# Performance work log

Hardware: AMD Instinct MI355X
Metric: run time of the kernel (lower is better)

## Reference

```python
import jax, jax.numpy as jnp
import numpy as np

LN_EPS = 1e-12


def setup_inputs() -> dict:
    key = jax.random.key(0)
    ks = jax.random.split(key, 5)
    E, H, I = 8, 768, 3072
    T = 2048  # tokens per expert (capacity-balanced)
    N = E * T
    return {
        "hidden_states": jax.random.normal(ks[0], (N, H), jnp.float32),
        "w1": jax.random.normal(ks[1], (E, H, I), jnp.float32) * (H ** -0.5),
        "b1": jax.random.normal(ks[2], (E, I), jnp.float32) * 0.02,
        "w2": jax.random.normal(ks[3], (E, I, H), jnp.float32) * (I ** -0.5),
        "b2": jax.random.normal(ks[4], (E, H), jnp.float32) * 0.02,
        "ln_gamma": jnp.ones((H,), jnp.float32),
        "ln_beta": jnp.zeros((H,), jnp.float32),
        "tokens_per_expert": T,
    }


def reference(hidden_states, w1, b1, w2, b2, ln_gamma, ln_beta, tokens_per_expert):
    E = w1.shape[0]
    N, H = hidden_states.shape
    # tokens are pre-sorted by expert; equal capacity per expert -> grouped GEMM
    x = hidden_states.reshape(E, tokens_per_expert, H)  # [E, T, H]
    # dense1 + exact GELU (BERT ACT2FN['gelu'])
    inter = jax.nn.gelu(jnp.einsum("eth,ehi->eti", x, w1) + b1[:, None, :],
                        approximate=False)  # [E, T, I]
    # dense2
    out = jnp.einsum("eti,eih->eth", inter, w2) + b2[:, None, :]  # [E, T, H]
    # dropout is identity in eval mode; residual + LayerNorm
    y = out.reshape(N, H) + hidden_states
    mean = jnp.mean(y, axis=-1, keepdims=True)
    var = jnp.mean(jnp.square(y - mean), axis=-1, keepdims=True)
    return (y - mean) * jax.lax.rsqrt(var + LN_EPS) * ln_gamma + ln_beta
```

## Files before the change

kernel.cpp:

```cpp
#include <hip/hip_runtime.h>
#include <hip/hip_bf16.h>
#include <math.h>

#define E_   8
#define H_   768
#define I_   3072
#define T_   2048
#define NTOK (E_ * T_)

typedef __attribute__((ext_vector_type(8))) short bf16x8;
typedef __attribute__((ext_vector_type(4))) float f32x4;

typedef __attribute__((address_space(3))) void lds_void;
typedef const __attribute__((address_space(1))) void gl_void;

__device__ __forceinline__ void gload16(const void* g, void* l) {
  __builtin_amdgcn_global_load_lds((gl_void*)g, (lds_void*)l, 16, 0, 0);
}

#define FENCE() asm volatile("" ::: "memory")
#define BAR()                         \
  do {                                \
    FENCE();                          \
    __builtin_amdgcn_s_barrier();     \
    FENCE();                          \
  } while (0)
#define VMWAIT(n) asm volatile("s_waitcnt vmcnt(" #n ")" ::: "memory")

#define MFMA16(a, b, c) __builtin_amdgcn_mfma_f32_16x16x32_bf16(a, b, c, 0, 0, 0)

__device__ __forceinline__ float gelu_fast(float v) {
  float inner = v * fmaf(v * v, 0.044715f, 1.0f);
  float e = __builtin_amdgcn_exp2f(inner * -2.3022082f);
  return v * __builtin_amdgcn_rcpf(1.0f + e);
}

__global__ __launch_bounds__(256) void cvt_bf16_kernel(
    const float* __restrict__ in, __hip_bfloat16* __restrict__ out) {
  int i = (blockIdx.x * 256 + threadIdx.x) * 4;
  float4 v = *(const float4*)(in + i);
  __align__(8) __hip_bfloat16 t[4];
  t[0] = __float2bfloat16(v.x);
  t[1] = __float2bfloat16(v.y);
  t[2] = __float2bfloat16(v.z);
  t[3] = __float2bfloat16(v.w);
  *(ushort4*)(out + i) = *(const ushort4*)t;
}

__global__ __launch_bounds__(256) void transpose_cvt_kernel(
    const float* __restrict__ src, __hip_bfloat16* __restrict__ dst,
    int R, int C) {
  __shared__ __hip_bfloat16 tile[64][65];
  int e  = blockIdx.z;
  int c0 = blockIdx.x * 64;
  int r0 = blockIdx.y * 64;
  const float* s = src + (size_t)e * R * C;
  __hip_bfloat16* d = dst + (size_t)e * R * C;
  int tx = threadIdx.x & 63, ty = threadIdx.x >> 6;
#pragma unroll
  for (int r = ty; r < 64; r += 4)
    tile[r][tx] = __float2bfloat16(s[(size_t)(r0 + r) * C + c0 + tx]);
  __syncthreads();
#pragma unroll
  for (int r = ty; r < 64; r += 4)
    d[(size_t)(c0 + r) * R + r0 + tx] = tile[tx][r];
}

template <int K, int N, int BN, bool GELU>
__global__ __launch_bounds__(512, 2) void gemm2p_kernel(
    const __hip_bfloat16* __restrict__ A,
    const __hip_bfloat16* __restrict__ B,
    const float* __restrict__ bias,
    __hip_bfloat16* __restrict__ out) {
  constexpr int MT = T_ / 256;
  constexpr int NT = N / BN;
  constexpr int KT = K / 64;
  constexpr int NF = BN / 64;
  constexpr int WCW = BN / 4;
  constexpr int BPASS = BN / 64;

  __shared__ __hip_bfloat16 sA[2][2][128][64];
  __shared__ __hip_bfloat16 sB[2][BN][64];

  int nwg = gridDim.x;
  int b0  = blockIdx.x;
  int bid = (b0 & 7) * (nwg >> 3) + (b0 >> 3);

  int e   = bid / (MT * NT);
  int rr_ = bid % (MT * NT);
  int bm  = rr_ / NT;
  int bn  = rr_ % NT;

  const __hip_bfloat16* Ae = A + (size_t)e * T_ * K + (size_t)bm * 256 * K;
  const __hip_bfloat16* Be = B + (size_t)e * N  * K + (size_t)bn * BN * K;

  int tid  = threadIdx.x;
  int lane = tid & 63;
  int wid  = tid >> 6;
  int wr   = wid >> 2;
  int wc   = wid & 3;
  int l15  = lane & 15;
  int l16h = lane >> 4;

  int i0 = tid, i1 = 512 + tid;
  int lr0 = i0 >> 3, c80 = i0 & 7, cg0 = c80 ^ (lr0 & 7);
  int lr1 = i1 >> 3, c81 = i1 & 7, cg1 = c81 ^ (lr1 & 7);
  int rA0 = ((lr0 >> 6) << 7) | (lr0 & 63);
  int rA1 = ((lr1 >> 6) << 7) | (lr1 & 63);

  auto stageA = [&](int buf, int h, int kt) {
    const __hip_bfloat16* g = Ae + (size_t)kt * 64;
    gload16(g + (size_t)(rA0 | (h << 6)) * K + cg0 * 8, &sA[buf][h][lr0][c80 * 8]);
    gload16(g + (size_t)(rA1 | (h << 6)) * K + cg1 * 8, &sA[buf][h][lr1][c81 * 8]);
  };
  auto stageB = [&](int buf, int kt) {
    const __hip_bfloat16* g = Be + (size_t)kt * 64;
#pragma unroll
    for (int q = 0; q < BPASS; ++q) {
      int idx = q * 512 + tid;
      int lr = idx >> 3, c8 = idx & 7;
      int cg = c8 ^ (lr & 7);
      gload16(g + (size_t)lr * K + cg * 8, &sB[buf][lr][c8 * 8]);
    }
  };

  int laBase = wr * 64 + l15;
  int lbBase = wc * WCW + l15;
  int s7   = l15 & 7;
  int cgr0 = ((0 | l16h) ^ s7) * 8;
  int cgr1 = ((4 | l16h) ^ s7) * 8;

  f32x4 acc[8][NF] = {};
  bf16x8 af[4][2], bfv[NF][2];

  stageA(0, 0, 0);
  stageB(0, 0);
  stageA(0, 1, 0);

  auto ktile = [&](int kt, int p, bool pf) {
    VMWAIT(2);
    BAR();
#pragma unroll
    for (int mf = 0; mf < 4; ++mf) {
      int la = laBase + mf * 16;
      af[mf][0] = *(const bf16x8*)&sA[p][0][la][cgr0];
      af[mf][1] = *(const bf16x8*)&sA[p][0][la][cgr1];
    }
#pragma unroll
    for (int nf = 0; nf < NF; ++nf) {
      int lb = lbBase + nf * 16;
      bfv[nf][0] = *(const bf16x8*)&sB[p][lb][cgr0];
      bfv[nf][1] = *(const bf16x8*)&sB[p][lb][cgr1];
    }
    if (pf) {
      stageA(p ^ 1, 0, kt + 1);
      stageB(p ^ 1, kt + 1);
    }
    __builtin_amdgcn_s_setprio(1);
#pragma unroll
    for (int mf = 0; mf < 4; ++mf)
#pragma unroll
      for (int nf = 0; nf < NF; ++nf) {
        acc[mf][nf] = MFMA16(af[mf][0], bfv[nf][0], acc[mf][nf]);
        acc[mf][nf] = MFMA16(af[mf][1], bfv[nf][1], acc[mf][nf]);
      }
    __builtin_amdgcn_s_setprio(0);
    if (pf) {
      if constexpr (BN == 256) { VMWAIT(6); } else { VMWAIT(5); }
    } else {
      VMWAIT(0);
    }
    BAR();
#pragma unroll
    for (int mf = 0; mf < 4; ++mf) {
      int la = laBase + mf * 16;
      af[mf][0] = *(const bf16x8*)&sA[p][1][la][cgr0];
      af[mf][1] = *(const bf16x8*)&sA[p][1][la][cgr1];
    }
    if (pf) stageA(p ^ 1, 1, kt + 1);
    __builtin_amdgcn_s_setprio(1);
#pragma unroll
    for (int mf = 0; mf < 4; ++mf)
#pragma unroll
      for (int nf = 0; nf < NF; ++nf) {
        acc[4 + mf][nf] = MFMA16(af[mf][0], bfv[nf][0], acc[4 + mf][nf]);
        acc[4 + mf][nf] = MFMA16(af[mf][1], bfv[nf][1], acc[4 + mf][nf]);
      }
    __builtin_amdgcn_s_setprio(0);
  };

  int p = 0;
  for (int kt = 0; kt < KT - 1; ++kt) {
    ktile(kt, p, true);
    p ^= 1;
  }
  ktile(KT - 1, p, false);

  const float* be = bias + (size_t)e * N + bn * BN;
  __hip_bfloat16* oe =
      out + (size_t)e * T_ * N + (size_t)(bm * 256) * N + bn * BN;
  int r4 = l16h * 4;
#pragma unroll
  for (int mi = 0; mi < 8; ++mi) {
    int mh = mi >> 2, mf = mi & 3;
    int rowb = wr * 128 + mh * 64 + mf * 16 + r4;
#pragma unroll
    for (int nf = 0; nf < NF; ++nf) {
      int cc   = wc * WCW + nf * 16 + l15;
      float bv = be[cc];
#pragma unroll
      for (int r = 0; r < 4; ++r) {
        float v = acc[mi][nf][r] + bv;
        if (GELU) v = gelu_fast(v);
        oe[(size_t)(rowb + r) * N + cc] = __float2bfloat16(v);
      }
    }
  }
}

__global__ __launch_bounds__(256) void ln_kernel(
    const __hip_bfloat16* __restrict__ yraw, const float* __restrict__ x,
    const float* __restrict__ gamma, const float* __restrict__ beta,
    float* __restrict__ out) {
  int row  = blockIdx.x;
  int tid  = threadIdx.x;
  int lane = tid & 63, wid = tid >> 6;
  const __hip_bfloat16* yr = yraw + (size_t)row * H_;
  const float* xr = x + (size_t)row * H_;

  float v[3];
  float s = 0.f, s2 = 0.f;
#pragma unroll
  for (int j = 0; j < 3; ++j) {
    int c   = tid + j * 256;
    float t = __bfloat162float(yr[c]) + xr[c];
    v[j] = t;
    s += t;
    s2 += t * t;
  }
#pragma unroll
  for (int o = 32; o > 0; o >>= 1) {
    s  += __shfl_down(s, o);
    s2 += __shfl_down(s2, o);
  }
  __shared__ float ls[4], ls2[4];
  if (lane == 0) { ls[wid] = s; ls2[wid] = s2; }
  __syncthreads();
  float tot  = ls[0] + ls[1] + ls[2] + ls[3];
  float tot2 = ls2[0] + ls2[1] + ls2[2] + ls2[3];
  float mean = tot * (1.0f / 768.0f);
  float var  = tot2 * (1.0f / 768.0f) - mean * mean;
  float inv  = rsqrtf(var + 1e-12f);
  float* orow = out + (size_t)row * H_;
#pragma unroll
  for (int j = 0; j < 3; ++j) {
    int c = tid + j * 256;
    orow[c] = (v[j] - mean) * inv * gamma[c] + beta[c];
  }
}

extern "C" void kernel_launch(void* const* d_in, const int* in_sizes, int n_in,
                              void* d_out, int out_size, void* d_ws,
                              size_t ws_size, hipStream_t stream) {
  const float* x     = (const float*)d_in[0];
  const float* w1    = (const float*)d_in[1];
  const float* b1    = (const float*)d_in[2];
  const float* w2    = (const float*)d_in[3];
  const float* b2    = (const float*)d_in[4];
  const float* gamma = (const float*)d_in[5];
  const float* beta  = (const float*)d_in[6];
  float* out = (float*)d_out;

  char* ws = (char*)d_ws;
  __hip_bfloat16* w1t   = (__hip_bfloat16*)(ws);
  __hip_bfloat16* w2t   = (__hip_bfloat16*)(ws + 37748736);
  __hip_bfloat16* x_bf  = (__hip_bfloat16*)(ws + 75497472);
  __hip_bfloat16* inter = (__hip_bfloat16*)(ws + 100663296);
  __hip_bfloat16* yraw  = x_bf;

  cvt_bf16_kernel<<<(NTOK * H_) / (256 * 4), 256, 0, stream>>>(x, x_bf);
  transpose_cvt_kernel<<<dim3(I_ / 64, H_ / 64, E_), 256, 0, stream>>>(
      w1, w1t, H_, I_);
  transpose_cvt_kernel<<<dim3(H_ / 64, I_ / 64, E_), 256, 0, stream>>>(
      w2, w2t, I_, H_);
  gemm2p_kernel<H_, I_, 256, true>
      <<<E_ * (T_ / 256) * (I_ / 256), 512, 0, stream>>>(x_bf, w1t, b1, inter);
  gemm2p_kernel<I_, H_, 192, false>
      <<<E_ * (T_ / 256) * (H_ / 192), 512, 0, stream>>>(inter, w2t, b2, yraw);
  ln_kernel<<<NTOK, 256, 0, stream>>>(yraw, x, gamma, beta, out);
}
```

Before: 252.8 us.

## Vectorize transpose, precompute GEMM load offsets, LayerNorm on bf16 residual

The weight transpose-convert kernel now does float2 loads and paired bf16 stores, with a padded tile. The GEMM staging lambdas use per-thread global and LDS offsets computed once, instead of redoing index math on every k-tile. LayerNorm uses 384 threads with two elements each and vector loads. It reads the bf16 copy of the input as the residual rather than the fp32 original, which roughly halves that read traffic but adds rounding error to the residual. The second GEMM's output now goes into the spent w1t buffer, so x_bf stays intact for this.

```diff
diff --git a/kernel.cpp b/kernel.cpp
--- a/kernel.cpp
+++ b/kernel.cpp
@@ -50,20 +50,32 @@
 __global__ __launch_bounds__(256) void transpose_cvt_kernel(
     const float* __restrict__ src, __hip_bfloat16* __restrict__ dst,
     int R, int C) {
-  __shared__ __hip_bfloat16 tile[64][65];
+  __shared__ __hip_bfloat16 tile[64][66];
   int e  = blockIdx.z;
   int c0 = blockIdx.x * 64;
   int r0 = blockIdx.y * 64;
   const float* s = src + (size_t)e * R * C;
   __hip_bfloat16* d = dst + (size_t)e * R * C;
-  int tx = threadIdx.x & 63, ty = threadIdx.x >> 6;
-#pragma unroll
-  for (int r = ty; r < 64; r += 4)
-    tile[r][tx] = __float2bfloat16(s[(size_t)(r0 + r) * C + c0 + tx]);
+  int tx = threadIdx.x & 31;
+  int ty = threadIdx.x >> 5;
+#pragma unroll
+  for (int r = ty; r < 64; r += 8) {
+    float2 v = *(const float2*)&s[(size_t)(r0 + r) * C + c0 + 2 * tx];
+    __hip_bfloat16 b0 = __float2bfloat16(v.x);
+    __hip_bfloat16 b1 = __float2bfloat16(v.y);
+    ushort2 w;
+    w.x = *(const ushort*)&b0;
+    w.y = *(const ushort*)&b1;
+    *(ushort2*)&tile[r][2 * tx] = w;
+  }
   __syncthreads();
 #pragma unroll
-  for (int r = ty; r < 64; r += 4)
-    d[(size_t)(c0 + r) * R + r0 + tx] = tile[tx][r];
+  for (int rr = ty; rr < 64; rr += 8) {
+    ushort2 v;
+    v.x = *(const ushort*)&tile[2 * tx][rr];
+    v.y = *(const ushort*)&tile[2 * tx + 1][rr];
+    *(ushort2*)&d[(size_t)(c0 + rr) * R + r0 + 2 * tx] = v;
+  }
 }
 
 template <int K, int N, int BN, bool GELU>
@@ -107,21 +119,30 @@
   int lr1 = i1 >> 3, c81 = i1 & 7, cg1 = c81 ^ (lr1 & 7);
   int rA0 = ((lr0 >> 6) << 7) | (lr0 & 63);
   int rA1 = ((lr1 >> 6) << 7) | (lr1 & 63);
+  const size_t oA0 = (size_t)rA0 * K + cg0 * 8;
+  const size_t oA1 = (size_t)rA1 * K + cg1 * 8;
+  const size_t HOFF = (size_t)64 * K;
+  size_t oB[BPASS];
+  int    dB[BPASS];
+#pragma unroll
+  for (int q = 0; q < BPASS; ++q) {
+    int idx = q * 512 + tid;
+    int lr = idx >> 3, c8 = idx & 7;
+    int cg = c8 ^ (lr & 7);
+    oB[q] = (size_t)lr * K + cg * 8;
+    dB[q] = lr * 64 + c8 * 8;
+  }
 
   auto stageA = [&](int buf, int h, int kt) {
-    const __hip_bfloat16* g = Ae + (size_t)kt * 64;
-    gload16(g + (size_t)(rA0 | (h << 6)) * K + cg0 * 8, &sA[buf][h][lr0][c80 * 8]);
-    gload16(g + (size_t)(rA1 | (h << 6)) * K + cg1 * 8, &sA[buf][h][lr1][c81 * 8]);
+    const __hip_bfloat16* g = Ae + (size_t)kt * 64 + (size_t)h * HOFF;
+    gload16(g + oA0, &sA[buf][h][lr0][c80 * 8]);
+    gload16(g + oA1, &sA[buf][h][lr1][c81 * 8]);
   };
   auto stageB = [&](int buf, int kt) {
     const __hip_bfloat16* g = Be + (size_t)kt * 64;
-#pragma unroll
-    for (int q = 0; q < BPASS; ++q) {
-      int idx = q * 512 + tid;
-      int lr = idx >> 3, c8 = idx & 7;
-      int cg = c8 ^ (lr & 7);
-      gload16(g + (size_t)lr * K + cg * 8, &sB[buf][lr][c8 * 8]);
-    }
+    __hip_bfloat16* l = &sB[buf][0][0];
+#pragma unroll
+    for (int q = 0; q < BPASS; ++q) gload16(g + oB[q], l + dB[q]);
   };
 
   int laBase = wr * 64 + l15;
@@ -218,45 +239,47 @@
   }
 }
 
-__global__ __launch_bounds__(256) void ln_kernel(
-    const __hip_bfloat16* __restrict__ yraw, const float* __restrict__ x,
+__global__ __launch_bounds__(384) void ln_kernel(
+    const __hip_bfloat16* __restrict__ yraw,
+    const __hip_bfloat16* __restrict__ xbf,
     const float* __restrict__ gamma, const float* __restrict__ beta,
     float* __restrict__ out) {
   int row  = blockIdx.x;
   int tid  = threadIdx.x;
   int lane = tid & 63, wid = tid >> 6;
+  int c    = tid * 2;
   const __hip_bfloat16* yr = yraw + (size_t)row * H_;
-  const float* xr = x + (size_t)row * H_;
-
-  float v[3];
-  float s = 0.f, s2 = 0.f;
-#pragma unroll
-  for (int j = 0; j < 3; ++j) {
-    int c   = tid + j * 256;
-    float t = __bfloat162float(yr[c]) + xr[c];
-    v[j] = t;
-    s += t;
-    s2 += t * t;
-  }
+  const __hip_bfloat16* xr = xbf + (size_t)row * H_;
+
+  ushort2 ya = *(const ushort2*)&yr[c];
+  ushort2 xa = *(const ushort2*)&xr[c];
+  __hip_bfloat16 t;
+  float v0, v1;
+  *(ushort*)&t = ya.x; v0 = __bfloat162float(t);
+  *(ushort*)&t = xa.x; v0 += __bfloat162float(t);
+  *(ushort*)&t = ya.y; v1 = __bfloat162float(t);
+  *(ushort*)&t = xa.y; v1 += __bfloat162float(t);
+
+  float s = v0 + v1, s2 = v0 * v0 + v1 * v1;
 #pragma unroll
   for (int o = 32; o > 0; o >>= 1) {
     s  += __shfl_down(s, o);
     s2 += __shfl_down(s2, o);
   }
-  __shared__ float ls[4], ls2[4];
+  __shared__ float ls[6], ls2[6];
   if (lane == 0) { ls[wid] = s; ls2[wid] = s2; }
   __syncthreads();
-  float tot  = ls[0] + ls[1] + ls[2] + ls[3];
-  float tot2 = ls2[0] + ls2[1] + ls2[2] + ls2[3];
+  float tot  = ls[0] + ls[1] + ls[2] + ls[3] + ls[4] + ls[5];
+  float tot2 = ls2[0] + ls2[1] + ls2[2] + ls2[3] + ls2[4] + ls2[5];
   float mean = tot * (1.0f / 768.0f);
   float var  = tot2 * (1.0f / 768.0f) - mean * mean;
   float inv  = rsqrtf(var + 1e-12f);
-  float* orow = out + (size_t)row * H_;
-#pragma unroll
-  for (int j = 0; j < 3; ++j) {
-    int c = tid + j * 256;
-    orow[c] = (v[j] - mean) * inv * gamma[c] + beta[c];
-  }
+  float2 g = *(const float2*)&gamma[c];
+  float2 b = *(const float2*)&beta[c];
+  float2 o2;
+  o2.x = (v0 - mean) * inv * g.x + b.x;
+  o2.y = (v1 - mean) * inv * g.y + b.y;
+  *(float2*)&out[(size_t)row * H_ + c] = o2;
 }
 
 extern "C" void kernel_launch(void* const* d_in, const int* in_sizes, int n_in,
@@ -276,7 +299,7 @@
   __hip_bfloat16* w2t   = (__hip_bfloat16*)(ws + 37748736);
   __hip_bfloat16* x_bf  = (__hip_bfloat16*)(ws + 75497472);
   __hip_bfloat16* inter = (__hip_bfloat16*)(ws + 100663296);
-  __hip_bfloat16* yraw  = x_bf;
+  __hip_bfloat16* yraw  = (__hip_bfloat16*)(ws);
 
   cvt_bf16_kernel<<<(NTOK * H_) / (256 * 4), 256, 0, stream>>>(x, x_bf);
   transpose_cvt_kernel<<<dim3(I_ / 64, H_ / 64, E_), 256, 0, stream>>>(
@@ -287,5 +310,5 @@
       <<<E_ * (T_ / 256) * (I_ / 256), 512, 0, stream>>>(x_bf, w1t, b1, inter);
   gemm2p_kernel<I_, H_, 192, false>
       <<<E_ * (T_ / 256) * (H_ / 192), 512, 0, stream>>>(inter, w2t, b2, yraw);
-  ln_kernel<<<NTOK, 256, 0, stream>>>(yraw, x, gamma, beta, out);
-}
+  ln_kernel<<<NTOK, 384, 0, stream>>>(yraw, x_bf, gamma, beta, out);
+}
```

New measurement: 242.1 us. 4.2% less time.
